# Kernel tuning notes

Measured on AMD Instinct MI355X. Metric: run time of the kernel, lower is better.

## Reference

```python
import jax, jax.numpy as jnp
import numpy as np

B, S, D = 4, 2048, 512
H, KD, VD = 8, 64, 64


def glorot(key, shape):
    fan_in, fan_out = shape[-2], shape[-1]
    limit = np.sqrt(6.0 / (fan_in + fan_out)).astype(np.float32)
    return jax.random.uniform(key, shape, jnp.float32, -limit, limit)


def setup_inputs() -> dict:
    key = jax.random.key(0)
    ks = jax.random.split(key, 6)
    input_tensor = jax.random.normal(ks[0], (B, S, D), jnp.float32)
    input_mask = jnp.ones((B, S), jnp.float32)
    # Per-head projections stacked along a leading head axis [H, D, kd/vd]
    Wq = glorot(ks[1], (H, D, KD))
    Wk = glorot(ks[2], (H, D, KD))
    Wv = glorot(ks[3], (H, D, VD))
    Wo = glorot(ks[4], (H * VD, VD))
    # dot_product_scales initialized to 1 in the original (tf.Variable(1))
    scales = jnp.ones((H,), jnp.float32)
    return {"input_tensor": input_tensor, "input_mask": input_mask,
            "Wq": Wq, "Wk": Wk, "Wv": Wv, "Wo": Wo, "scales": scales}


def reference(input_tensor, input_mask, Wq, Wk, Wv, Wo, scales):
    # Vectorized over the original per-head Python loop (identical math).
    q = jnp.einsum('bsd,hdk->bhsk', input_tensor, Wq)
    k = jnp.einsum('bsd,hdk->bhsk', input_tensor, Wk)
    v = jnp.einsum('bsd,hdv->bhsv', input_tensor, Wv)
    # dotproduct notation 'bik,bjk->bij' per head, scaled by per-head scale
    scores = jnp.einsum('bhik,bhjk->bhij', q, k) * scales[None, :, None, None]
    # reshape to [..., -1] then softmax == softmax over last (key) axis here
    attn = jax.nn.softmax(scores, axis=-1)
    # kv notation 'bij,bjv,bi,bj->biv' with the mask applied twice
    ctx = jnp.einsum('bhij,bhjv,bi,bj->bhiv', attn, v, input_mask, input_mask)
    # concat heads along last axis (head-major order, as in the loop)
    ctx = jnp.transpose(ctx, (0, 2, 1, 3)).reshape(ctx.shape[0], ctx.shape[2], -1)
    return ctx @ Wo
```

## Files before the change

### kernel.cpp

```cpp
#include <hip/hip_runtime.h>
#include <hip/hip_bf16.h>


typedef _Float16 f16x8 __attribute__((ext_vector_type(8)));
typedef float    f32x4  __attribute__((ext_vector_type(4)));
typedef float    f32x16 __attribute__((ext_vector_type(16)));
typedef __fp16   hf2 __attribute__((ext_vector_type(2)));

#define BB 4
#define SS 2048
#define DD 512
#define HH 8
#define KDIM 64
#define NSPLIT 4
#define TPS 8

#define EXP2F(x) __builtin_amdgcn_exp2f(x)

#define GLOAD_LDS16(gp, lp)                                                   \
  __builtin_amdgcn_global_load_lds(                                          \
      (const __attribute__((address_space(1))) void*)(gp),                    \
      (__attribute__((address_space(3))) void*)(lp), 16, 0, 0)

#define SWZ(row, bc) ((row) * 128 + ((bc) ^ (((row) & 7) << 4)))

static __device__ __forceinline__ unsigned pk2(float a, float b) {
  auto h = __builtin_amdgcn_cvt_pkrtz(a, b);
  return __builtin_bit_cast(unsigned, h);
}

union PU { unsigned u[4]; f16x8 v; };

__global__ __launch_bounds__(256) void convert_x(
    const float* __restrict__ x, _Float16* __restrict__ xf) {
  size_t i = ((size_t)blockIdx.x * 256 + threadIdx.x) * 8;
  float4 a = *(const float4*)&x[i];
  float4 b = *(const float4*)&x[i + 4];
  float vv[8] = {a.x, a.y, a.z, a.w, b.x, b.y, b.z, b.w};
  _Float16 hb[8];
#pragma unroll
  for (int u = 0; u < 8; ++u) hb[u] = (_Float16)vv[u];
  *(uint4*)&xf[i] = *(uint4*)hb;
}

__global__ __launch_bounds__(256) void convert_w(
    const float* __restrict__ Wq, const float* __restrict__ Wk,
    const float* __restrict__ Wv, _Float16* __restrict__ wtf) {
  __shared__ float s_tile[64][65];
  const int t = threadIdx.x;
  const int kb = blockIdx.x;
  const int hw = blockIdx.y;
  const int which = hw >> 3, h = hw & 7;
  const float* W = (which == 0) ? Wq : (which == 1) ? Wk : Wv;
  const float* src = W + (size_t)h * DD * KDIM + (size_t)kb * 64 * KDIM;

  {
    int kk = t >> 2, c0 = (t & 3) * 16;
#pragma unroll
    for (int u = 0; u < 4; ++u)
      *(float4*)&s_tile[kk][c0 + u * 4] = *(const float4*)&src[kk * KDIM + c0 + u * 4];
  }
  __syncthreads();

  int kd = t >> 2, kk0 = (t & 3) * 16;
  int n = which * 512 + h * 64 + kd;
  _Float16 hb[16];
#pragma unroll
  for (int u = 0; u < 16; ++u) hb[u] = (_Float16)s_tile[kk0 + u][kd];
  size_t off = (size_t)n * DD + kb * 64 + kk0;
  *(uint4*)&wtf[off] = *(uint4*)&hb[0];
  *(uint4*)&wtf[off + 8] = *(uint4*)&hb[8];
}

__global__ __launch_bounds__(256) void convert_wo(
    const float* __restrict__ Wo, _Float16* __restrict__ woT) {
  __shared__ float s_tile[64][65];
  const int t = threadIdx.x;
  const int kb = blockIdx.x;
  const float* src = Wo + (size_t)kb * 64 * 64;
  {
    int kk = t >> 2, c0 = (t & 3) * 16;
#pragma unroll
    for (int u = 0; u < 4; ++u)
      *(float4*)&s_tile[kk][c0 + u * 4] = *(const float4*)&src[kk * 64 + c0 + u * 4];
  }
  __syncthreads();
  int col = t >> 2, kk0 = (t & 3) * 16;
  _Float16 hb[16];
#pragma unroll
  for (int u = 0; u < 16; ++u) hb[u] = (_Float16)s_tile[kk0 + u][col];
  size_t off = (size_t)col * DD + kb * 64 + kk0;
  *(uint4*)&woT[off] = *(uint4*)&hb[0];
  *(uint4*)&woT[off + 8] = *(uint4*)&hb[8];
}

__global__ __launch_bounds__(256) void qkv_gemm(
    const _Float16* __restrict__ xf, const _Float16* __restrict__ wtf,
    const float* __restrict__ mask, const float* __restrict__ scales,
    _Float16* __restrict__ qf, _Float16* __restrict__ kf,
    _Float16* __restrict__ vT) {
  __shared__ _Float16 Af[128 * 32], Bf[128 * 32];
  const int t = threadIdx.x, l = t & 63, w = t >> 6;
  const int wr = w >> 1, wc = w & 1;
  const int m0 = blockIdx.y * 128, n0 = blockIdx.x * 128;

  f32x4 acc[4][4];
#pragma unroll
  for (int m = 0; m < 4; ++m)
#pragma unroll
    for (int n = 0; n < 4; ++n) acc[m][n] = f32x4{0.f, 0.f, 0.f, 0.f};

  const int rl = l >> 2, ce = (l & 3) * 8;

  for (int kt = 0; kt < 16; ++kt) {
    const int k0 = kt * 32;
    __syncthreads();
#pragma unroll
    for (int i = 0; i < 2; ++i) {
      const int row = w * 32 + i * 16;
      const size_t aoff = (size_t)(m0 + row + rl) * DD + k0 + ce;
      const size_t boff = (size_t)(n0 + row + rl) * DD + k0 + ce;
      GLOAD_LDS16(xf + aoff, &Af[row * 32]);
      GLOAD_LDS16(wtf + boff, &Bf[row * 32]);
    }
    __syncthreads();

    f16x8 ah[4], bh[4];
#pragma unroll
    for (int m = 0; m < 4; ++m) {
      int r = wr * 64 + m * 16 + (l & 15);
      ah[m] = *(const f16x8*)&Af[r * 32 + (l >> 4) * 8];
    }
#pragma unroll
    for (int n = 0; n < 4; ++n) {
      int r = wc * 64 + n * 16 + (l & 15);
      bh[n] = *(const f16x8*)&Bf[r * 32 + (l >> 4) * 8];
    }
#pragma unroll
    for (int m = 0; m < 4; ++m)
#pragma unroll
      for (int n = 0; n < 4; ++n)
        acc[m][n] = __builtin_amdgcn_mfma_f32_16x16x32_f16(ah[m], bh[n], acc[m][n], 0, 0, 0);
  }

#pragma unroll
  for (int n = 0; n < 4; ++n) {
    int colg = n0 + wc * 64 + n * 16 + (l & 15);
    int which = colg >> 9, rem = colg & 511;
    int h = rem >> 6, kd = rem & 63;
    float qsc = (which == 0) ? scales[h] * 1.44269504f : 1.f;
#pragma unroll
    for (int m = 0; m < 4; ++m) {
      int row0 = m0 + wr * 64 + m * 16 + (l >> 4) * 4;
      if (which == 2) {
        int b = row0 >> 11, s0 = row0 & 2047;
        _Float16 tmp[4] __attribute__((aligned(8)));
#pragma unroll
        for (int j = 0; j < 4; ++j)
          tmp[j] = (_Float16)(acc[m][n][j] * mask[row0 + j]);
        *(uint2*)&vT[((size_t)(b * HH + h) * KDIM + kd) * SS + s0] = *(uint2*)tmp;
      } else {
        _Float16* dst = (which == 0) ? qf : kf;
#pragma unroll
        for (int j = 0; j < 4; ++j) {
          int row = row0 + j;
          int b = row >> 11, s = row & 2047;
          dst[(((size_t)b * HH + h) * SS + s) * KDIM + kd] =
              (_Float16)(acc[m][n][j] * qsc);
        }
      }
    }
  }
}

__global__ __launch_bounds__(256) void attn_kernel(
    const _Float16* __restrict__ qg, const _Float16* __restrict__ kg,
    const _Float16* __restrict__ vTg,
    _Float16* __restrict__ po, float* __restrict__ pli) {
  const int t = threadIdx.x;
  const int l = t & 63, w = t >> 6;
  const int lr = l & 31, hi = l >> 5;
  const int bh = blockIdx.y;
  const int q0 = blockIdx.x * 128;
  const int split = blockIdx.z;

  __shared__ _Float16 ksf[64 * 64];
  __shared__ _Float16 vts[64 * 64];

  const size_t base = (size_t)bh * SS * KDIM;
  const size_t vbase = (size_t)bh * KDIM * SS;

  f16x8 qfr[4];
  const int s_q = q0 + w * 32 + lr;
#pragma unroll
  for (int kb = 0; kb < 4; ++kb)
    qfr[kb] = *(const f16x8*)&qg[base + (size_t)s_q * KDIM + kb * 16 + hi * 8];

  float m_s = -1e30f, lsum = 0.f;
  f32x16 oacc[2] = {};

  const int kt0 = split * TPS;
  for (int kt = kt0; kt < kt0 + TPS; ++kt) {
    __syncthreads();
#pragma unroll
    for (int c = 0; c < 2; ++c) {
      const int r = w * 16 + c * 8 + (l >> 3);
      const int ecol = ((l & 7) * 8) ^ (((l >> 3) & 7) * 8);
      size_t koff = base + (size_t)(kt * 64 + r) * KDIM + ecol;
      size_t voff = vbase + (size_t)r * SS + kt * 64 + ecol;
      GLOAD_LDS16(kg + koff, ksf + (w * 16 + c * 8) * 64);
      GLOAD_LDS16(vTg + voff, vts + (w * 16 + c * 8) * 64);
    }
    __syncthreads();

    f32x16 st2[2];
#pragma unroll
    for (int jb = 0; jb < 2; ++jb) {
      f32x16 acc = {};
      const int krow = jb * 32 + lr;
#pragma unroll
      for (int kb = 0; kb < 4; ++kb) {
        f16x8 kfr = *(const f16x8*)((const char*)ksf + SWZ(krow, kb * 32 + hi * 16));
        acc = __builtin_amdgcn_mfma_f32_32x32x16_f16(kfr, qfr[kb], acc, 0, 0, 0);
      }
      st2[jb] = acc;
    }

    float m8[8];
#pragma unroll
    for (int i = 0; i < 8; ++i)
      m8[i] = fmaxf(fmaxf(st2[0][i], st2[0][i + 8]),
                    fmaxf(st2[1][i], st2[1][i + 8]));
    float m4a = fmaxf(m8[0], m8[1]), m4b = fmaxf(m8[2], m8[3]);
    float m4c = fmaxf(m8[4], m8[5]), m4d = fmaxf(m8[6], m8[7]);
    float mt = fmaxf(fmaxf(m4a, m4b), fmaxf(m4c, m4d));
    mt = fmaxf(mt, __shfl_xor(mt, 32, 64));

    if (!__all(mt <= m_s + 11.5f)) {
      float mn = fmaxf(m_s, mt);
      float rs = EXP2F(m_s - mn);
      m_s = mn;
      lsum *= rs;
#pragma unroll
      for (int nb = 0; nb < 2; ++nb)
#pragma unroll
        for (int rr = 0; rr < 16; ++rr) oacc[nb][rr] *= rs;
    }

    float ps0 = 0.f, ps1 = 0.f;
    unsigned wds[2][4][2];
#pragma unroll
    for (int jb = 0; jb < 2; ++jb)
#pragma unroll
      for (int g = 0; g < 4; ++g) {
        float p0 = EXP2F(st2[jb][g * 4 + 0] - m_s);
        float p1 = EXP2F(st2[jb][g * 4 + 1] - m_s);
        float p2 = EXP2F(st2[jb][g * 4 + 2] - m_s);
        float p3 = EXP2F(st2[jb][g * 4 + 3] - m_s);
        unsigned pa = pk2(p0, p1), pb = pk2(p2, p3);
        wds[jb][g][0] = pa;
        wds[jb][g][1] = pb;
#if __has_builtin(__builtin_amdgcn_fdot2)
        hf2 one2 = {(__fp16)1.f, (__fp16)1.f};
        ps0 = __builtin_amdgcn_fdot2(__builtin_bit_cast(hf2, pa), one2, ps0, false);
        ps1 = __builtin_amdgcn_fdot2(__builtin_bit_cast(hf2, pb), one2, ps1, false);
#else
        ps0 += p0 + p1;
        ps1 += p2 + p3;
#endif
      }
    float psum = ps0 + ps1;
    psum += __shfl_xor(psum, 32, 64);
    lsum += psum;

#pragma unroll
    for (int kb = 0; kb < 4; ++kb) {
      const int jb = kb >> 1, gb = (kb & 1) * 2;
      unsigned s0 = hi ? wds[jb][gb][0] : wds[jb][gb + 1][0];
      unsigned s1 = hi ? wds[jb][gb][1] : wds[jb][gb + 1][1];
      unsigned r0 = (unsigned)__shfl_xor((int)s0, 32, 64);
      unsigned r1 = (unsigned)__shfl_xor((int)s1, 32, 64);
      PU pu;
      pu.u[0] = hi ? r0 : wds[jb][gb][0];
      pu.u[1] = hi ? r1 : wds[jb][gb][1];
      pu.u[2] = hi ? wds[jb][gb + 1][0] : r0;
      pu.u[3] = hi ? wds[jb][gb + 1][1] : r1;
#pragma unroll
      for (int nb = 0; nb < 2; ++nb) {
        f16x8 vf = *(const f16x8*)((const char*)vts + SWZ(nb * 32 + lr, kb * 32 + hi * 16));
        oacc[nb] = __builtin_amdgcn_mfma_f32_32x32x16_f16(vf, pu.v, oacc[nb], 0, 0, 0);
      }
    }
  }

  const float inv = 1.0f / lsum;
  const float li = m_s + __log2f(lsum);
  _Float16* prow = po + (((size_t)split * (BB * HH) + bh) * SS + s_q) * KDIM;
#pragma unroll
  for (int nb = 0; nb < 2; ++nb)
#pragma unroll
    for (int g = 0; g < 4; ++g) {
      uint2 o;
      o.x = pk2(oacc[nb][g * 4 + 0] * inv, oacc[nb][g * 4 + 1] * inv);
      o.y = pk2(oacc[nb][g * 4 + 2] * inv, oacc[nb][g * 4 + 3] * inv);
      *(uint2*)&prow[nb * 32 + g * 8 + hi * 4] = o;
    }
  if (hi == 0)
    pli[((size_t)split * (BB * HH) + bh) * SS + s_q] = li;
}

__global__ __launch_bounds__(256) void attn_combine(
    const _Float16* __restrict__ po, const float* __restrict__ pli,
    const float* __restrict__ mask, _Float16* __restrict__ ctxf) {
  const int t = threadIdx.x;
  const int row = blockIdx.x * 32 + (t >> 3);
  const int c = t & 7;
  const int bh = row >> 11, qrow = row & 2047;
  const int b = bh >> 3, h = bh & 7;
  const int NR = BB * HH * SS;

  float li[NSPLIT];
#pragma unroll
  for (int s = 0; s < NSPLIT; ++s) li[s] = pli[(size_t)s * NR + row];
  float L = fmaxf(fmaxf(li[0], li[1]), fmaxf(li[2], li[3]));
  float wgt[NSPLIT], wsum = 0.f;
#pragma unroll
  for (int s = 0; s < NSPLIT; ++s) { wgt[s] = EXP2F(li[s] - L); wsum += wgt[s]; }

  float acc[8] = {};
#pragma unroll
  for (int s = 0; s < NSPLIT; ++s) {
    uint4 u = *(const uint4*)&po[((size_t)s * NR + row) * KDIM + c * 8];
    const _Float16* hp = (const _Float16*)&u;
#pragma unroll
    for (int j = 0; j < 8; ++j) acc[j] += wgt[s] * (float)hp[j];
  }
  const float sc = mask[b * SS + qrow] / wsum;
  _Float16 ob[8] __attribute__((aligned(16)));
#pragma unroll
  for (int j = 0; j < 8; ++j) ob[j] = (_Float16)(acc[j] * sc);
  *(uint4*)&ctxf[((size_t)b * SS + qrow) * (HH * KDIM) + h * KDIM + c * 8] =
      *(uint4*)ob;
}

__global__ __launch_bounds__(256) void oproj_gemm(
    const _Float16* __restrict__ ctxf, const _Float16* __restrict__ woT,
    float* __restrict__ out) {
  __shared__ _Float16 Af[64 * 32], Bf[64 * 32];
  const int t = threadIdx.x, l = t & 63, w = t >> 6;
  const int lr = l & 31, hi = l >> 5;
  const int wr = w >> 1, wc = w & 1;
  const size_t rowbase = (size_t)blockIdx.x * 64;
  const int rl = l >> 2, ce = (l & 3) * 8;

  f32x16 acc = {};
  for (int kt = 0; kt < 16; ++kt) {
    const int k0 = kt * 32;
    __syncthreads();
    {
      const int row = w * 16;
      GLOAD_LDS16(ctxf + (rowbase + row + rl) * DD + k0 + ce, &Af[row * 32]);
      GLOAD_LDS16(woT + (size_t)(row + rl) * DD + k0 + ce, &Bf[row * 32]);
    }
    __syncthreads();
#pragma unroll
    for (int ks = 0; ks < 2; ++ks) {
      f16x8 af = *(const f16x8*)&Af[(wr * 32 + lr) * 32 + ks * 16 + hi * 8];
      f16x8 bf = *(const f16x8*)&Bf[(wc * 32 + lr) * 32 + ks * 16 + hi * 8];
      acc = __builtin_amdgcn_mfma_f32_32x32x16_f16(af, bf, acc, 0, 0, 0);
    }
  }
#pragma unroll
  for (int rr = 0; rr < 16; ++rr) {
    int m = (rr & 3) + 8 * (rr >> 2) + 4 * hi;
    out[(rowbase + wr * 32 + m) * 64 + wc * 32 + lr] = acc[rr];
  }
}

extern "C" void kernel_launch(void* const* d_in, const int* in_sizes, int n_in,
                              void* d_out, int out_size, void* d_ws, size_t ws_size,
                              hipStream_t stream) {
  const float* x     = (const float*)d_in[0];
  const float* mask  = (const float*)d_in[1];
  const float* Wq    = (const float*)d_in[2];
  const float* Wk    = (const float*)d_in[3];
  const float* Wv    = (const float*)d_in[4];
  const float* Wo    = (const float*)d_in[5];
  const float* scales= (const float*)d_in[6];
  float* out = (float*)d_out;

  char* ws = (char*)d_ws;
  const size_t xb  = (size_t)BB * SS * DD * sizeof(_Float16);
  const size_t wb  = (size_t)3 * 512 * DD * sizeof(_Float16);
  const size_t wob = (size_t)64 * DD * sizeof(_Float16);
  const size_t qb  = (size_t)BB * HH * SS * KDIM * sizeof(_Float16);
  const size_t pob = (size_t)NSPLIT * BB * HH * SS * KDIM * sizeof(_Float16);
  const size_t plib= (size_t)NSPLIT * BB * HH * SS * sizeof(float);

  _Float16* xfb  = (_Float16*)(ws);
  _Float16* wtfb = (_Float16*)(ws + xb);
  _Float16* woTb = (_Float16*)(ws + xb + wb);
  char* p = ws + xb + wb + wob;
  _Float16* qfb  = (_Float16*)(p);
  _Float16* kfb  = (_Float16*)(p + qb);
  _Float16* vTb  = (_Float16*)(p + 2 * qb);
  _Float16* ctxf = (_Float16*)(p + 3 * qb);
  _Float16* pob_p= (_Float16*)(p + 4 * qb);
  float*    pli_p= (float*)(p + 4 * qb + pob);
  (void)plib; (void)ws_size;

  convert_x<<<2048, 256, 0, stream>>>(x, xfb);
  convert_w<<<dim3(8, 24), 256, 0, stream>>>(Wq, Wk, Wv, wtfb);
  convert_wo<<<8, 256, 0, stream>>>(Wo, woTb);
  qkv_gemm<<<dim3(12, 64), 256, 0, stream>>>(xfb, wtfb, mask, scales,
                                             qfb, kfb, vTb);
  attn_kernel<<<dim3(SS / 128, BB * HH, NSPLIT), 256, 0, stream>>>(
      qfb, kfb, vTb, pob_p, pli_p);
  attn_combine<<<(BB * HH * SS) / 32, 256, 0, stream>>>(pob_p, pli_p, mask, ctxf);
  oproj_gemm<<<128, 256, 0, stream>>>(ctxf, woTb, out);
}
```

Measured before the change: 121.2 us.

## Double-buffer K/V tiles in attention and halve the key-split count

The attention kernel now keeps two LDS buffers for K and V and issues the async global-to-LDS loads for the next key tile while computing on the current one. This replaces the two barriers per iteration with one at the end of each iteration. The split-K factor drops from 4 to 2, giving each block twice as many tiles to amortise the prologue and halving the partial-output traffic into the combine kernel. The cost is fewer blocks in the grid (1024 instead of 2048), which lowers parallelism and occupancy, plus double the LDS per block.

```diff
diff --git a/kernel.cpp b/kernel.cpp
--- a/kernel.cpp
+++ b/kernel.cpp
@@ -12,8 +12,8 @@
 #define DD 512
 #define HH 8
 #define KDIM 64
-#define NSPLIT 4
-#define TPS 8
+#define NSPLIT 2
+#define TPS 16
 
 #define EXP2F(x) __builtin_amdgcn_exp2f(x)
 
@@ -184,12 +184,15 @@
   const int q0 = blockIdx.x * 128;
   const int split = blockIdx.z;
 
-  __shared__ _Float16 ksf[64 * 64];
-  __shared__ _Float16 vts[64 * 64];
+  __shared__ _Float16 ksf[2][64 * 64];
+  __shared__ _Float16 vts[2][64 * 64];
 
   const size_t base = (size_t)bh * SS * KDIM;
   const size_t vbase = (size_t)bh * KDIM * SS;
 
+  const int srow = l >> 3;
+  const int ecol = ((l & 7) * 8) ^ ((srow & 7) * 8);
+
   f16x8 qfr[4];
   const int s_q = q0 + w * 32 + lr;
 #pragma unroll
@@ -200,18 +203,30 @@
   f32x16 oacc[2] = {};
 
   const int kt0 = split * TPS;
-  for (int kt = kt0; kt < kt0 + TPS; ++kt) {
-    __syncthreads();
-#pragma unroll
-    for (int c = 0; c < 2; ++c) {
-      const int r = w * 16 + c * 8 + (l >> 3);
-      const int ecol = ((l & 7) * 8) ^ (((l >> 3) & 7) * 8);
-      size_t koff = base + (size_t)(kt * 64 + r) * KDIM + ecol;
-      size_t voff = vbase + (size_t)r * SS + kt * 64 + ecol;
-      GLOAD_LDS16(kg + koff, ksf + (w * 16 + c * 8) * 64);
-      GLOAD_LDS16(vTg + voff, vts + (w * 16 + c * 8) * 64);
-    }
-    __syncthreads();
+
+#pragma unroll
+  for (int c = 0; c < 2; ++c) {
+    const int r = w * 16 + c * 8 + srow;
+    GLOAD_LDS16(kg + base + (size_t)(kt0 * 64 + r) * KDIM + ecol,
+                &ksf[0][(w * 16 + c * 8) * 64]);
+    GLOAD_LDS16(vTg + vbase + (size_t)r * SS + kt0 * 64 + ecol,
+                &vts[0][(w * 16 + c * 8) * 64]);
+  }
+  __syncthreads();
+
+  for (int tt = 0; tt < TPS; ++tt) {
+    const int cur = tt & 1;
+    if (tt + 1 < TPS) {
+      const int ktn = kt0 + tt + 1;
+#pragma unroll
+      for (int c = 0; c < 2; ++c) {
+        const int r = w * 16 + c * 8 + srow;
+        GLOAD_LDS16(kg + base + (size_t)(ktn * 64 + r) * KDIM + ecol,
+                    &ksf[1 - cur][(w * 16 + c * 8) * 64]);
+        GLOAD_LDS16(vTg + vbase + (size_t)r * SS + ktn * 64 + ecol,
+                    &vts[1 - cur][(w * 16 + c * 8) * 64]);
+      }
+    }
 
     f32x16 st2[2];
 #pragma unroll
@@ -220,7 +235,7 @@
       const int krow = jb * 32 + lr;
 #pragma unroll
       for (int kb = 0; kb < 4; ++kb) {
-        f16x8 kfr = *(const f16x8*)((const char*)ksf + SWZ(krow, kb * 32 + hi * 16));
+        f16x8 kfr = *(const f16x8*)((const char*)&ksf[cur][0] + SWZ(krow, kb * 32 + hi * 16));
         acc = __builtin_amdgcn_mfma_f32_32x32x16_f16(kfr, qfr[kb], acc, 0, 0, 0);
       }
       st2[jb] = acc;
@@ -287,10 +302,12 @@
       pu.u[3] = hi ? wds[jb][gb + 1][1] : r1;
 #pragma unroll
       for (int nb = 0; nb < 2; ++nb) {
-        f16x8 vf = *(const f16x8*)((const char*)vts + SWZ(nb * 32 + lr, kb * 32 + hi * 16));
+        f16x8 vf = *(const f16x8*)((const char*)&vts[cur][0] + SWZ(nb * 32 + lr, kb * 32 + hi * 16));
         oacc[nb] = __builtin_amdgcn_mfma_f32_32x32x16_f16(vf, pu.v, oacc[nb], 0, 0, 0);
       }
     }
+
+    __syncthreads();
   }
 
   const float inv = 1.0f / lsum;
@@ -322,7 +339,9 @@
   float li[NSPLIT];
 #pragma unroll
   for (int s = 0; s < NSPLIT; ++s) li[s] = pli[(size_t)s * NR + row];
-  float L = fmaxf(fmaxf(li[0], li[1]), fmaxf(li[2], li[3]));
+  float L = li[0];
+#pragma unroll
+  for (int s = 1; s < NSPLIT; ++s) L = fmaxf(L, li[s]);
   float wgt[NSPLIT], wsum = 0.f;
 #pragma unroll
   for (int s = 0; s < NSPLIT; ++s) { wgt[s] = EXP2F(li[s] - L); wsum += wgt[s]; }
@@ -395,7 +414,6 @@
   const size_t wob = (size_t)64 * DD * sizeof(_Float16);
   const size_t qb  = (size_t)BB * HH * SS * KDIM * sizeof(_Float16);
   const size_t pob = (size_t)NSPLIT * BB * HH * SS * KDIM * sizeof(_Float16);
-  const size_t plib= (size_t)NSPLIT * BB * HH * SS * sizeof(float);
 
   _Float16* xfb  = (_Float16*)(ws);
   _Float16* wtfb = (_Float16*)(ws + xb);
@@ -407,7 +425,7 @@
   _Float16* ctxf = (_Float16*)(p + 3 * qb);
   _Float16* pob_p= (_Float16*)(p + 4 * qb);
   float*    pli_p= (float*)(p + 4 * qb + pob);
-  (void)plib; (void)ws_size;
+  (void)ws_size;
 
   convert_x<<<2048, 256, 0, stream>>>(x, xfb);
   convert_w<<<dim3(8, 24), 256, 0, stream>>>(Wq, Wk, Wv, wtfb);
```

After: 123.9 us. 2.2% more time.
